# Kernel tuning notes

Hardware: AMD Instinct MI355X
Metric: run time of the kernel (lower is better)

Reference implementation:

```python
import jax, jax.numpy as jnp
import numpy as np

N = 50000   # nodes per graph
E = 400000  # edges per graph (avg degree 8)
L = 16      # regex token length per edge
V = 64      # VOCAB_SIZE
EMB = 32    # REGEX_EMBEDDING_DIMENSION
H = 128     # LSTM_DIMENSION
D = 373     # hidden_vector_dim (MAX_STATES=50)
IN_IDX = 161
OUT_IDX = 320
SID = 53    # MAX_STATES + 3
SLOPE = 0.2 # GATv2 leaky_relu negative slope

def _lstm_cell(x_t, h, c, Wih, Whh, b):
    g = x_t @ Wih.T + h @ Whh.T + b          # [E, 4H], torch gate order i,f,g,o
    i, f, gg, o = jnp.split(g, 4, axis=-1)
    c = jax.nn.sigmoid(f) * c + jax.nn.sigmoid(i) * jnp.tanh(gg)
    h = jax.nn.sigmoid(o) * jnp.tanh(c)
    return h, c

def _edge_scalar(tokens, embed, Wih_f, Whh_f, b_f, Wih_r, Whh_r, b_r, W1, b1, W2, b2):
    emb = embed.at[0].set(0.0)[tokens]       # padding_idx=0; [E, L, EMB]
    En = tokens.shape[0]
    h0 = jnp.zeros((En, H), jnp.float32)
    def step(carry, x_t):
        h, c = _lstm_cell(x_t, carry[0], carry[1], Wih_f, Whh_f, b_f)
        return (h, c), None
    (h_fwd, _), _ = jax.lax.scan(step, (h0, h0), jnp.swapaxes(emb, 0, 1))
    # bidirectional output at last timestep: reverse direction has consumed only token L-1
    h_bwd, _ = _lstm_cell(emb[:, -1], h0, h0, Wih_r, Whh_r, b_r)
    feat = jax.nn.relu(jnp.concatenate([h_fwd, h_bwd], axis=-1) @ W1 + b1)
    return jax.nn.relu(feat @ W2 + b2)[:, 0]  # [E]

def _gatv2(x, src, dst, Wl, bl, Wr, br, att, bias):
    xl = x @ Wl + bl                          # source transform (messages)
    xr = x @ Wr + br                          # target transform
    m = jax.nn.leaky_relu(xl[src] + xr[dst], SLOPE)  # [E, D]
    e = m @ att                                      # [E]
    e_max = jax.ops.segment_max(e, dst, num_segments=N)
    ex = jnp.exp(e - e_max[dst])
    denom = jax.ops.segment_sum(ex, dst, num_segments=N)
    alpha = ex / (denom[dst] + 1e-16)                # scatter-softmax over in-edges
    agg = jax.ops.segment_sum(alpha[:, None] * xl[src], dst, num_segments=N)
    return agg + bias

def _process(x, ei, edge_attr, Wl, bl, Wr, br, att, bias):
    src, dst = ei[0], ei[1]
    src_id = jnp.argmax(x[src, :SID], axis=-1)
    tgt_id = jnp.argmax(x[dst, :SID], axis=-1)
    x = x.at[dst, IN_IDX + src_id].set(edge_attr)   # index_put scatter writes
    x = x.at[src, OUT_IDX + tgt_id].set(edge_attr)
    return jax.nn.relu(_gatv2(x, src, dst, Wl, bl, Wr, br, att, bias) + x)

def setup_inputs():
    key = jax.random.key(0)
    ks = jax.random.split(key, 40)
    rn = lambda k, s, sc=0.05: jax.random.normal(k, s, dtype=jnp.float32) * sc
    return {
        "fx": jax.random.normal(ks[0], (N, D), dtype=jnp.float32),
        "bx": jax.random.normal(ks[1], (N, D), dtype=jnp.float32),
        "f_edge_index": jax.random.randint(ks[2], (2, E), 0, N),
        "b_edge_index": jax.random.randint(ks[3], (2, E), 0, N),
        "f_tokens": jax.random.randint(ks[4], (E, L), 0, V),
        "b_tokens": jax.random.randint(ks[5], (E, L), 0, V),
        "embed": rn(ks[6], (V, EMB), 1.0),
        "Wih_f": rn(ks[7], (4 * H, EMB)),
        "Whh_f": rn(ks[8], (4 * H, H)),
        "bih_f": rn(ks[9], (4 * H,)),
        "bhh_f": rn(ks[10], (4 * H,)),
        "Wih_r": rn(ks[11], (4 * H, EMB)),
        "Whh_r": rn(ks[12], (4 * H, H)),
        "bih_r": rn(ks[13], (4 * H,)),
        "bhh_r": rn(ks[14], (4 * H,)),
        "W1": rn(ks[15], (2 * H, 32)),
        "b1": rn(ks[16], (32,)),
        "W2": rn(ks[17], (32, 1)),
        "b2": rn(ks[18], (1,)),
        "fWl": rn(ks[19], (D, D)), "fbl": rn(ks[20], (D,)),
        "fWr": rn(ks[21], (D, D)), "fbr": rn(ks[22], (D,)),
        "fatt": rn(ks[23], (D,)), "fbias": rn(ks[24], (D,)),
        "bWl": rn(ks[25], (D, D)), "bbl": rn(ks[26], (D,)),
        "bWr": rn(ks[27], (D, D)), "bbr": rn(ks[28], (D,)),
        "batt": rn(ks[29], (D,)), "bbias": rn(ks[30], (D,)),
    }

def reference(fx, bx, f_edge_index, b_edge_index, f_tokens, b_tokens, embed,
              Wih_f, Whh_f, bih_f, bhh_f, Wih_r, Whh_r, bih_r, bhh_r,
              W1, b1, W2, b2,
              fWl, fbl, fWr, fbr, fatt, fbias,
              bWl, bbl, bWr, bbr, batt, bbias):
    b_f = bih_f + bhh_f
    b_r = bih_r + bhh_r
    f_ea = _edge_scalar(f_tokens, embed, Wih_f, Whh_f, b_f, Wih_r, Whh_r, b_r, W1, b1, W2, b2)
    b_ea = _edge_scalar(b_tokens, embed, Wih_f, Whh_f, b_f, Wih_r, Whh_r, b_r, W1, b1, W2, b2)
    fxo = _process(fx, f_edge_index, f_ea, fWl, fbl, fWr, fbr, fatt, fbias)
    bxo = _process(bx, b_edge_index, b_ea, bWl, bbl, bWr, bbr, batt, bbias)
    return jnp.concatenate([fxo, bxo], axis=-1)  # [N, 2*D]
```

## Files before the change

### kernel.cpp

```cpp
#include <hip/hip_runtime.h>
#include <cstdint>


#define D_DIM   373
#define SID_N   53
#define IN_COL  161
#define OUT_COL 320
#define HS_STRIDE 136
#define EDGES_T 64
#define N_ES    4

typedef short bf16x8 __attribute__((ext_vector_type(8)));
typedef float f32x4  __attribute__((ext_vector_type(4)));

#define LOG2E_F 1.4426950408889634f
#define TWO_LOG2E_F 2.8853900817779268f

__device__ __forceinline__ float fast_exp2(float x) {
#if __has_builtin(__builtin_amdgcn_exp2f)
  return __builtin_amdgcn_exp2f(x);
#else
  return exp2f(x);
#endif
}
__device__ __forceinline__ float fast_rcp(float x) {
#if __has_builtin(__builtin_amdgcn_rcpf)
  return __builtin_amdgcn_rcpf(x);
#else
  return 1.0f / x;
#endif
}
__device__ __forceinline__ float sig_ref(float x)  { return 1.0f / (1.0f + __expf(-x)); }
__device__ __forceinline__ float tanh_ref(float x) { return 2.0f / (1.0f + __expf(-2.0f * x)) - 1.0f; }

__device__ __forceinline__ unsigned short f2bf(float f) {
  unsigned u = __float_as_uint(f);
  unsigned r = (u + 0x7fffu + ((u >> 16) & 1u)) >> 16;
  return (unsigned short)r;
}
__device__ __forceinline__ float bflo2f(unsigned u) { return __uint_as_float(u << 16); }
__device__ __forceinline__ float bfhi2f(unsigned u) { return __uint_as_float(u & 0xffff0000u); }
__device__ __forceinline__ unsigned cvt_pk_bf16(float lo, float hi) {
  unsigned r;
  asm("v_cvt_pk_bf16_f32 %0, %1, %2" : "=v"(r) : "v"(lo), "v"(hi));
  return r;
}
__device__ __forceinline__ float pair_sig_tanh(float A, float B) {
  return (B - 1.0f) * fast_rcp((1.0f + A) * (1.0f + B));
}

__global__ void fill_u32_kernel(unsigned* __restrict__ p, unsigned v, size_t n) {
  size_t i = (size_t)blockIdx.x * blockDim.x + threadIdx.x;
  size_t stride = (size_t)gridDim.x * blockDim.x;
  for (; i < n; i += stride) p[i] = v;
}

__global__ void precompute_kernel(
    const float* __restrict__ embed, const float* __restrict__ Wih_f,
    const float* __restrict__ Whh_f,
    const float* __restrict__ bih_f, const float* __restrict__ bhh_f,
    const float* __restrict__ Wih_r,
    const float* __restrict__ bih_r, const float* __restrict__ bhh_r,
    const float* __restrict__ W1, const float* __restrict__ b1,
    unsigned short* __restrict__ Pg, unsigned short* __restrict__ BfragW,
    unsigned short* __restrict__ Bfrag1, float* __restrict__ FB)
{
  __shared__ float ps[512];
  __shared__ float gb[512];
  __shared__ float hb[128];
  int v = blockIdx.x;
  int j = threadIdx.x;

  float s = 0.0f;
  if (v != 0) {
    #pragma unroll
    for (int k = 0; k < 32; ++k) s += embed[v * 32 + k] * Wih_f[j * 32 + k];
  }
  ps[j] = s + bih_f[j] + bhh_f[j];

  float gr = bih_r[j] + bhh_r[j];
  if (v != 0) {
    #pragma unroll
    for (int k = 0; k < 32; ++k) gr += embed[v * 32 + k] * Wih_r[j * 32 + k];
  }
  gb[j] = gr;
  __syncthreads();
  if (j < 128) {
    float c = sig_ref(gb[j]) * tanh_ref(gb[256 + j]);
    hb[j] = sig_ref(gb[384 + j]) * tanh_ref(c);
  }
  __syncthreads();

  { int h = j >> 2, g = j & 3;
    float sc = (g == 2) ? TWO_LOG2E_F : -LOG2E_F;
    Pg[((size_t)v * 128 + h) * 4 + g] = f2bf(ps[g * 128 + h] * sc); }

  if (j < 32) {
    float s2 = b1[j];
    for (int m = 0; m < 128; ++m) s2 += hb[m] * W1[(128 + m) * 32 + j];
    FB[v * 32 + j] = s2;
  }

  if (v == 0) {
    for (int f = j; f < 65536; f += 512) {
      int e = f & 7, l = (f >> 3) & 63, ks = (f >> 9) & 3, nt = f >> 11;
      int n = nt * 16 + (l & 15);
      int k = ks * 32 + (l >> 4) * 8 + e;
      float sc = ((nt >> 3) == 2) ? TWO_LOG2E_F : -LOG2E_F;
      BfragW[f] = f2bf(Whh_f[(size_t)n * 128 + k] * sc);
    }
  }
  if (v == 1) {
    for (int f = j; f < 4096; f += 512) {
      int e = f & 7, l = (f >> 3) & 63, ks = (f >> 9) & 3, n2 = f >> 11;
      int q = n2 * 16 + (l & 15);
      int k = ks * 32 + (l >> 4) * 8 + e;
      Bfrag1[f] = f2bf(W1[(size_t)k * 32 + q]);
    }
  }
}

__global__ __launch_bounds__(512, 4) void lstm_mfma_kernel(
    const int*   __restrict__ tokens,
    const unsigned short* __restrict__ Pg,
    const unsigned short* __restrict__ BfragW,
    const unsigned short* __restrict__ Bfrag1,
    const float* __restrict__ FB,
    const float* __restrict__ W2,
    const float* __restrict__ b2,
    float* __restrict__ ea, int E, int nTiles)
{
  __shared__ unsigned short Hs[2][EDGES_T * HS_STRIDE];
  __shared__ int toks[16][EDGES_T];

  int tid  = threadIdx.x;
  int lane = tid & 63;
  int wv2  = tid >> 6;
  int l15  = lane & 15;
  int lg   = lane >> 4;
  int hbase = wv2 * 16 + lg * 4;

  bf16x8 BW[4][4];
  #pragma unroll
  for (int gate = 0; gate < 4; ++gate)
    #pragma unroll
    for (int ks = 0; ks < 4; ++ks)
      BW[gate][ks] = *(const bf16x8*)(BfragW +
          ((size_t)((gate * 8 + wv2) * 4 + ks) * 64 + lane) * 8);

  for (int tile = blockIdx.x; tile < nTiles; tile += gridDim.x) {
    int e0 = tile * EDGES_T;
    for (int i = tid; i < 16 * EDGES_T; i += 512) {
      int m = i >> 4, t = i & 15;
      int ee = e0 + m; if (ee >= E) ee = E - 1;
      toks[t][m] = tokens[(size_t)ee * 16 + t];
    }
    __syncthreads();

    f32x4 cst[N_ES];
    #pragma unroll
    for (int es = 0; es < N_ES; ++es) {
      int eL = es * 16 + l15;
      int v0 = toks[0][eL];
      const uint4* pp = (const uint4*)(Pg + ((size_t)v0 * 128 + hbase) * 4);
      uint4 pa = pp[0], pb = pp[1];
      float pi[4] = {bflo2f(pa.x), bflo2f(pa.z), bflo2f(pb.x), bflo2f(pb.z)};
      float pg[4] = {bflo2f(pa.y), bflo2f(pa.w), bflo2f(pb.y), bflo2f(pb.w)};
      float po[4] = {bfhi2f(pa.y), bfhi2f(pa.w), bfhi2f(pb.y), bfhi2f(pb.w)};
      float h[4];
      #pragma unroll
      for (int r = 0; r < 4; ++r) {
        float A = fast_exp2(pi[r]);
        float B = fast_exp2(pg[r]);
        float O = fast_exp2(po[r]);
        float cn = pair_sig_tanh(A, B);
        cst[es][r] = cn;
        float C = fast_exp2(TWO_LOG2E_F * cn);
        h[r] = pair_sig_tanh(O, C);
      }
      uint2 hp = make_uint2(cvt_pk_bf16(h[0], h[1]), cvt_pk_bf16(h[2], h[3]));
      *(uint2*)(&Hs[0][eL * HS_STRIDE + hbase]) = hp;
    }
    __syncthreads();

    int cur = 0;
    #pragma unroll 1
    for (int t = 1; t < 16; ++t) {
      #pragma unroll
      for (int es = 0; es < N_ES; ++es) {
        int eL = es * 16 + l15;
        int vt = toks[t][eL];
        const uint4* pp = (const uint4*)(Pg + ((size_t)vt * 128 + hbase) * 4);
        uint4 pa = pp[0], pb = pp[1];
        f32x4 acc[4];
        acc[0] = (f32x4){bflo2f(pa.x), bflo2f(pa.z), bflo2f(pb.x), bflo2f(pb.z)};
        acc[1] = (f32x4){bfhi2f(pa.x), bfhi2f(pa.z), bfhi2f(pb.x), bfhi2f(pb.z)};
        acc[2] = (f32x4){bflo2f(pa.y), bflo2f(pa.w), bflo2f(pb.y), bflo2f(pb.w)};
        acc[3] = (f32x4){bfhi2f(pa.y), bfhi2f(pa.w), bfhi2f(pb.y), bfhi2f(pb.w)};

        #pragma unroll
        for (int ks = 0; ks < 4; ++ks) {
          bf16x8 Hf = *(const bf16x8*)(&Hs[cur][eL * HS_STRIDE + ks * 32 + lg * 8]);
          #pragma unroll
          for (int gate = 0; gate < 4; ++gate)
            acc[gate] = __builtin_amdgcn_mfma_f32_16x16x32_bf16(
                BW[gate][ks], Hf, acc[gate], 0, 0, 0);
        }

        float h[4];
        #pragma unroll
        for (int r = 0; r < 4; ++r) {
          float A = fast_exp2(acc[0][r]);
          float F = fast_exp2(acc[1][r]);
          float B = fast_exp2(acc[2][r]);
          float O = fast_exp2(acc[3][r]);
          float ig = pair_sig_tanh(A, B);
          float f  = fast_rcp(1.0f + F);
          float cn = fmaf(f, cst[es][r], ig);
          cst[es][r] = cn;
          float C = fast_exp2(TWO_LOG2E_F * cn);
          h[r] = pair_sig_tanh(O, C);
        }
        uint2 hp = make_uint2(cvt_pk_bf16(h[0], h[1]), cvt_pk_bf16(h[2], h[3]));
        *(uint2*)(&Hs[cur ^ 1][eL * HS_STRIDE + hbase]) = hp;
      }
      cur ^= 1;
      __syncthreads();
    }

    if (wv2 < N_ES) {
      int eL = wv2 * 16 + l15;
      bf16x8 Hf[4];
      #pragma unroll
      for (int ks = 0; ks < 4; ++ks)
        Hf[ks] = *(const bf16x8*)(&Hs[cur][eL * HS_STRIDE + ks * 32 + lg * 8]);
      f32x4 a2[2];
      a2[0] = (f32x4){0.f, 0.f, 0.f, 0.f};
      a2[1] = (f32x4){0.f, 0.f, 0.f, 0.f};
      #pragma unroll
      for (int ks = 0; ks < 4; ++ks)
        #pragma unroll
        for (int n2 = 0; n2 < 2; ++n2)
          a2[n2] = __builtin_amdgcn_mfma_f32_16x16x32_bf16(
              *(const bf16x8*)(Bfrag1 + ((size_t)(n2 * 4 + ks) * 64 + lane) * 8),
              Hf[ks], a2[n2], 0, 0, 0);
      float4 w2lo = *(const float4*)(W2 + lg * 4);
      float4 w2hi = *(const float4*)(W2 + 16 + lg * 4);
      float b2v = b2[0];
      int v15 = toks[15][eL];
      float4 fb0 = *(const float4*)(FB + v15 * 32 + lg * 4);
      float4 fb1 = *(const float4*)(FB + v15 * 32 + 16 + lg * 4);
      float pr = fmaxf(a2[0][0] + fb0.x, 0.f) * w2lo.x
               + fmaxf(a2[0][1] + fb0.y, 0.f) * w2lo.y
               + fmaxf(a2[0][2] + fb0.z, 0.f) * w2lo.z
               + fmaxf(a2[0][3] + fb0.w, 0.f) * w2lo.w
               + fmaxf(a2[1][0] + fb1.x, 0.f) * w2hi.x
               + fmaxf(a2[1][1] + fb1.y, 0.f) * w2hi.y
               + fmaxf(a2[1][2] + fb1.z, 0.f) * w2hi.z
               + fmaxf(a2[1][3] + fb1.w, 0.f) * w2hi.w;
      pr += __shfl_xor(pr, 16);
      pr += __shfl_xor(pr, 32);
      int eidx = e0 + eL;
      if (lane < 16 && eidx < E) ea[eidx] = fmaxf(pr + b2v, 0.0f);
    }
    __syncthreads();
  }
}

__global__ __launch_bounds__(256) void node_argmax_kernel(
    const float* __restrict__ x, int* __restrict__ nid, int N)
{
  int n = (blockIdx.x * 256 + threadIdx.x) >> 6;
  int lane = threadIdx.x & 63;
  if (n >= N) return;
  float v = (lane < SID_N) ? x[(size_t)n * D_DIM + lane] : -3.4e38f;
  int idx = lane;
  #pragma unroll
  for (int o = 32; o > 0; o >>= 1) {
    float ov = __shfl_down(v, o);
    int   oi = __shfl_down(idx, o);
    if (ov > v || (ov == v && oi < idx)) { v = ov; idx = oi; }
  }
  if (lane == 0) nid[n] = idx;
}

__global__ void edge_winner_kernel(
    const int* __restrict__ ei, const int* __restrict__ nid,
    int* __restrict__ win_in, int* __restrict__ win_out, int E)
{
  int e = blockIdx.x * 256 + threadIdx.x;
  if (e >= E) return;
  int s = ei[e];
  int t = ei[E + e];
  atomicMax(&win_in[(size_t)t * SID_N + nid[s]], e);
  atomicMax(&win_out[(size_t)s * SID_N + nid[t]], e);
}

__global__ void scatter_resolve_kernel(
    const int* __restrict__ ei, const int* __restrict__ nid,
    const float* __restrict__ ea,
    const int* __restrict__ win_in, const int* __restrict__ win_out,
    float* __restrict__ x_mod, int E)
{
  int e = blockIdx.x * 256 + threadIdx.x;
  if (e >= E) return;
  int s = ei[e];
  int t = ei[E + e];
  int sid = nid[s], tix = nid[t];
  if (win_in[(size_t)t * SID_N + sid] == e)
    x_mod[(size_t)t * D_DIM + IN_COL + sid] = ea[e];
  if (win_out[(size_t)s * SID_N + tix] == e)
    x_mod[(size_t)s * D_DIM + OUT_COL + tix] = ea[e];
}

__global__ void pack_w_kernel(const float* __restrict__ Wl,
                              const float* __restrict__ Wr,
                              unsigned short* __restrict__ Wfrag)
{
  int f = blockIdx.x * 256 + threadIdx.x;
  if (f >= 48 * 12 * 64 * 8) return;
  int e = f & 7, l = (f >> 3) & 63;
  int rest = f >> 9;
  int ks = rest % 12, nt = rest / 12;
  int nl = nt * 16 + (l & 15);
  int k  = ks * 32 + (l >> 4) * 8 + e;
  float val = 0.0f;
  if (k < D_DIM) {
    if (nl < D_DIM)                      val = Wl[(size_t)k * D_DIM + nl];
    else if (nl >= 384 && nl < 384 + D_DIM) val = Wr[(size_t)k * D_DIM + (nl - 384)];
  }
  Wfrag[f] = f2bf(val);
}

__global__ __launch_bounds__(256, 2) void gemm_mfma_kernel(
    const float* __restrict__ A,
    const unsigned short* __restrict__ Wfrag,
    const float* __restrict__ bl, const float* __restrict__ br,
    float* __restrict__ xl, float* __restrict__ xr, int N)
{
  __shared__ unsigned short As[64][40];
  int tid  = threadIdx.x;
  int lane = tid & 63;
  int wv   = tid >> 6;
  int l15  = lane & 15, lg = lane >> 4;
  int m0   = blockIdx.x * 64;
  int nt   = blockIdx.y * 4 + wv;

  f32x4 acc[4];
  #pragma unroll
  for (int i = 0; i < 4; ++i) acc[i] = (f32x4){0.f, 0.f, 0.f, 0.f};

  int srow = tid >> 2, seg = tid & 3;
  int gr = m0 + srow; if (gr >= N) gr = N - 1;
  const float* arow = A + (size_t)gr * D_DIM;

  for (int ks = 0; ks < 12; ++ks) {
    int c0 = ks * 32 + seg * 8;
    float v[8];
    #pragma unroll
    for (int j = 0; j < 8; ++j) v[j] = (c0 + j < D_DIM) ? arow[c0 + j] : 0.0f;
    unsigned pk0 = cvt_pk_bf16(v[0], v[1]);
    unsigned pk1 = cvt_pk_bf16(v[2], v[3]);
    unsigned pk2 = cvt_pk_bf16(v[4], v[5]);
    unsigned pk3 = cvt_pk_bf16(v[6], v[7]);
    __syncthreads();
    *(uint4*)(&As[srow][seg * 8]) = make_uint4(pk0, pk1, pk2, pk3);
    __syncthreads();

    bf16x8 Bf = *(const bf16x8*)(Wfrag + ((size_t)(nt * 12 + ks) * 64 + lane) * 8);
    #pragma unroll
    for (int msub = 0; msub < 4; ++msub) {
      bf16x8 Af = *(const bf16x8*)(&As[msub * 16 + l15][lg * 8]);
      acc[msub] = __builtin_amdgcn_mfma_f32_16x16x32_bf16(Af, Bf, acc[msub], 0, 0, 0);
    }
  }

  int nl = nt * 16 + l15;
  float* dst = nullptr; int col = 0; const float* bias_ = nullptr;
  if (nl < D_DIM)                         { dst = xl; col = nl;       bias_ = bl; }
  else if (nl >= 384 && nl < 384 + D_DIM) { dst = xr; col = nl - 384; bias_ = br; }
  if (dst) {
    float bv = bias_[col];
    #pragma unroll
    for (int msub = 0; msub < 4; ++msub) {
      #pragma unroll
      for (int r = 0; r < 4; ++r) {
        int m = m0 + msub * 16 + lg * 4 + r;
        if (m < N) dst[(size_t)m * D_DIM + col] = acc[msub][r] + bv;
      }
    }
  }
}

__global__ __launch_bounds__(256) void edge_e_kernel(
    const float* __restrict__ xl, const float* __restrict__ xr,
    const float* __restrict__ att, const int* __restrict__ ei,
    float* __restrict__ e_buf, int E)
{
  int widx = (blockIdx.x * 256 + threadIdx.x) >> 6;
  int lane = threadIdx.x & 63;
  if (widx >= E) return;
  int s = ei[widx], t = ei[E + widx];
  const float* pl = xl + (size_t)s * D_DIM;
  const float* pr = xr + (size_t)t * D_DIM;
  float acc = 0.0f;
  for (int d = lane; d < D_DIM; d += 64) {
    float m = pl[d] + pr[d];
    m = (m > 0.0f) ? m : 0.2f * m;
    acc += m * att[d];
  }
  #pragma unroll
  for (int o = 32; o > 0; o >>= 1) acc += __shfl_down(acc, o);
  if (lane == 0) e_buf[widx] = acc;
}

__global__ void hist_kernel(const int* __restrict__ ei, unsigned* __restrict__ deg,
                            int E) {
  int e = blockIdx.x * 256 + threadIdx.x;
  if (e >= E) return;
  atomicAdd(&deg[ei[E + e]], 1u);
}

__global__ void scan1_kernel(const unsigned* __restrict__ deg,
                             unsigned* __restrict__ excl,
                             unsigned* __restrict__ bsum, int n) {
  __shared__ unsigned s[256];
  int t = threadIdx.x;
  int i = blockIdx.x * 256 + t;
  unsigned v = (i < n) ? deg[i] : 0u;
  s[t] = v; __syncthreads();
  #pragma unroll
  for (int o = 1; o < 256; o <<= 1) {
    unsigned u = (t >= o) ? s[t - o] : 0u;
    __syncthreads();
    s[t] += u;
    __syncthreads();
  }
  if (i < n) excl[i] = s[t] - v;
  if (t == 255) bsum[blockIdx.x] = s[255];
}

__global__ void scan2_kernel(unsigned* __restrict__ bsum, int nb) {
  __shared__ unsigned s[256];
  int t = threadIdx.x;
  unsigned v = (t < nb) ? bsum[t] : 0u;
  s[t] = v; __syncthreads();
  #pragma unroll
  for (int o = 1; o < 256; o <<= 1) {
    unsigned u = (t >= o) ? s[t - o] : 0u;
    __syncthreads();
    s[t] += u;
    __syncthreads();
  }
  if (t < nb) bsum[t] = s[t] - v;
}

__global__ void scan3_kernel(unsigned* __restrict__ excl,
                             const unsigned* __restrict__ bsum, int n) {
  int i = blockIdx.x * 256 + threadIdx.x;
  if (i < n) excl[i] += bsum[i >> 8];
}

__global__ void place_kernel(const int* __restrict__ ei,
                             unsigned* __restrict__ offs,
                             int* __restrict__ csr_eid, int E) {
  int e = blockIdx.x * 256 + threadIdx.x;
  if (e >= E) return;
  unsigned j = atomicAdd(&offs[ei[E + e]], 1u);
  csr_eid[j] = e;
}

__global__ __launch_bounds__(256) void node_gat_kernel(
    const int* __restrict__ ei, const int* __restrict__ csr_eid,
    const unsigned* __restrict__ offs, const unsigned* __restrict__ deg,
    float* __restrict__ ebuf, const float* __restrict__ xl,
    const float* __restrict__ xmod, const float* __restrict__ bias,
    float* __restrict__ out, int N, int E, int goff)
{
  int n = (blockIdx.x * 256 + threadIdx.x) >> 6;
  int lane = threadIdx.x & 63;
  if (n >= N) return;
  unsigned end = offs[n], d = deg[n], start = end - d;

  float mx = -3.4e38f;
  for (unsigned j = start; j < end; ++j)
    mx = fmaxf(mx, ebuf[csr_eid[j]]);
  float den = 0.0f;
  for (unsigned j = start; j < end; ++j) {
    int eid = csr_eid[j];
    float ex = __expf(ebuf[eid] - mx);
    ebuf[eid] = ex;
    den += ex;
  }
  float inv = 1.0f / (den + 1e-16f);

  float o0 = 0, o1 = 0, o2 = 0, o3 = 0, o4 = 0, o5 = 0;
  for (unsigned j = start; j < end; ++j) {
    int eid = csr_eid[j];
    float w = ebuf[eid] * inv;
    const float* row = xl + (size_t)ei[eid] * D_DIM;
    o0 = fmaf(w, row[lane], o0);
    o1 = fmaf(w, row[64 + lane], o1);
    o2 = fmaf(w, row[128 + lane], o2);
    o3 = fmaf(w, row[192 + lane], o3);
    o4 = fmaf(w, row[256 + lane], o4);
    if (lane < 53) o5 = fmaf(w, row[320 + lane], o5);
  }

  const float* xm = xmod + (size_t)n * D_DIM;
  float* op = out + (size_t)n * (2 * D_DIM) + goff;
  op[lane]       = fmaxf(o0 + bias[lane]       + xm[lane],       0.0f);
  op[64 + lane]  = fmaxf(o1 + bias[64 + lane]  + xm[64 + lane],  0.0f);
  op[128 + lane] = fmaxf(o2 + bias[128 + lane] + xm[128 + lane], 0.0f);
  op[192 + lane] = fmaxf(o3 + bias[192 + lane] + xm[192 + lane], 0.0f);
  op[256 + lane] = fmaxf(o4 + bias[256 + lane] + xm[256 + lane], 0.0f);
  if (lane < 53)
    op[320 + lane] = fmaxf(o5 + bias[320 + lane] + xm[320 + lane], 0.0f);
}

extern "C" void kernel_launch(void* const* d_in, const int* in_sizes, int n_in,
                              void* d_out, int out_size, void* d_ws, size_t ws_size,
                              hipStream_t stream)
{
  const float* fx     = (const float*)d_in[0];
  const float* bx     = (const float*)d_in[1];
  const int*   fei    = (const int*)d_in[2];
  const int*   bei    = (const int*)d_in[3];
  const int*   ftk    = (const int*)d_in[4];
  const int*   btk    = (const int*)d_in[5];
  const float* embed  = (const float*)d_in[6];
  const float* Wih_f  = (const float*)d_in[7];
  const float* Whh_f  = (const float*)d_in[8];
  const float* bih_f  = (const float*)d_in[9];
  const float* bhh_f  = (const float*)d_in[10];
  const float* Wih_r  = (const float*)d_in[11];
  const float* bih_r  = (const float*)d_in[13];
  const float* bhh_r  = (const float*)d_in[14];
  const float* W1     = (const float*)d_in[15];
  const float* b1     = (const float*)d_in[16];
  const float* W2     = (const float*)d_in[17];
  const float* b2     = (const float*)d_in[18];

  const float* Wl_g[2]   = {(const float*)d_in[19], (const float*)d_in[25]};
  const float* bl_g[2]   = {(const float*)d_in[20], (const float*)d_in[26]};
  const float* Wr_g[2]   = {(const float*)d_in[21], (const float*)d_in[27]};
  const float* br_g[2]   = {(const float*)d_in[22], (const float*)d_in[28]};
  const float* att_g[2]  = {(const float*)d_in[23], (const float*)d_in[29]};
  const float* bias_g[2] = {(const float*)d_in[24], (const float*)d_in[30]};
  const float* x_g[2]    = {fx, bx};
  const int*   ei_g[2]   = {fei, bei};
  const int*   tk_g[2]   = {ftk, btk};

  const int E = in_sizes[2] / 2;
  const int N = in_sizes[0] / D_DIM;

  char* wsb = (char*)d_ws;
  size_t off = 0;
  auto alloc = [&](size_t bytes) -> void* {
    void* p = wsb + off; off += (bytes + 255) & ~(size_t)255; return p;
  };
  unsigned short* Pg     = (unsigned short*)alloc((size_t)64 * 128 * 4 * 2);
  unsigned short* BfragW = (unsigned short*)alloc((size_t)65536 * 2);
  unsigned short* Bfrag1 = (unsigned short*)alloc((size_t)4096 * 2);
  unsigned short* Wfrag2 = (unsigned short*)alloc((size_t)2 * 294912 * 2);
  float* FB    = (float*)alloc((size_t)64 * 32 * 4);
  float* ea    = (float*)alloc((size_t)E * 4);
  float* ebuf  = (float*)alloc((size_t)E * 4);
  int*   nid   = (int*)alloc((size_t)N * 4);
  int*   csr_eid = (int*)alloc((size_t)E * 4);
  unsigned* deg  = (unsigned*)alloc((size_t)N * 4);
  unsigned* offs = (unsigned*)alloc((size_t)N * 4);
  unsigned* bsum = (unsigned*)alloc((size_t)256 * 4);
  int* win_in  = (int*)alloc((size_t)N * SID_N * 4);
  int* win_out = (int*)alloc((size_t)N * SID_N * 4);
  float* xmod  = (float*)alloc((size_t)N * D_DIM * 4);
  float* xl    = (float*)alloc((size_t)N * D_DIM * 4);
  float* xr    = (float*)alloc((size_t)N * D_DIM * 4);
  (void)ws_size; (void)n_in; (void)out_size;

  const size_t win_u32 = (size_t)((char*)win_out - (char*)win_in) / 4
                         + (size_t)N * SID_N;

  float* out = (float*)d_out;

  precompute_kernel<<<64, 512, 0, stream>>>(
      embed, Wih_f, Whh_f, bih_f, bhh_f, Wih_r, bih_r, bhh_r, W1, b1,
      Pg, BfragW, Bfrag1, FB);
  pack_w_kernel<<<(294912 + 255) / 256, 256, 0, stream>>>(
      Wl_g[0], Wr_g[0], Wfrag2);
  pack_w_kernel<<<(294912 + 255) / 256, 256, 0, stream>>>(
      Wl_g[1], Wr_g[1], Wfrag2 + 294912);

  const int nTiles  = (E + EDGES_T - 1) / EDGES_T;
  const int gridL   = nTiles < 2048 ? nTiles : 2048;
  const int gridE   = (E + 255) / 256;
  const int gridEW  = (E + 3) / 4;
  const int nScanB  = (N + 255) / 256;
  const int gridNd  = (N * 64 + 255) / 256;
  dim3 gridG((N + 63) / 64, 12);

  for (int g = 0; g < 2; ++g) {
    const float* x  = x_g[g];
    const int*   ei = ei_g[g];

    lstm_mfma_kernel<<<gridL, 512, 0, stream>>>(tk_g[g], Pg, BfragW, Bfrag1,
                                                FB, W2, b2, ea, E, nTiles);

    hipMemcpyAsync(xmod, x, (size_t)N * D_DIM * sizeof(float),
                   hipMemcpyDeviceToDevice, stream);
    node_argmax_kernel<<<gridNd, 256, 0, stream>>>(x, nid, N);
    fill_u32_kernel<<<2048, 256, 0, stream>>>((unsigned*)win_in, 0xFFFFFFFFu,
                                              win_u32);
    edge_winner_kernel<<<gridE, 256, 0, stream>>>(ei, nid, win_in, win_out, E);
    scatter_resolve_kernel<<<gridE, 256, 0, stream>>>(ei, nid, ea,
                                                      win_in, win_out, xmod, E);

    gemm_mfma_kernel<<<gridG, 256, 0, stream>>>(xmod, Wfrag2 + (size_t)g * 294912,
                                                bl_g[g], br_g[g], xl, xr, N);

    fill_u32_kernel<<<512, 256, 0, stream>>>(deg, 0u, (size_t)N);
    hist_kernel<<<gridE, 256, 0, stream>>>(ei, deg, E);
    scan1_kernel<<<nScanB, 256, 0, stream>>>(deg, offs, bsum, N);
    scan2_kernel<<<1, 256, 0, stream>>>(bsum, nScanB);
    scan3_kernel<<<nScanB, 256, 0, stream>>>(offs, bsum, N);
    place_kernel<<<gridE, 256, 0, stream>>>(ei, offs, csr_eid, E);

    edge_e_kernel<<<gridEW, 256, 0, stream>>>(xl, xr, att_g[g], ei, ebuf, E);
    node_gat_kernel<<<gridNd, 256, 0, stream>>>(ei, csr_eid, offs, deg, ebuf,
                                                xl, xmod, bias_g[g], out,
                                                N, E, g * D_DIM);
  }
}
```

Before: 3.596 ms.

## Compute GAT edge scores per destination node via CSR, reuse target row

Replaces the per-edge attention-score kernel with a per-node kernel that walks each node's in-edges through the CSR. The target row xr[n] and the att vector are loaded into registers once per node instead of once per edge, cutting global reads. It also shrinks the LSTM edge tile from 64 to 48 edges (N_ES 4 to 3), which changes that kernel's occupancy and grid size. The cost is serial work per node, so load balance depends on the degree distribution.

Result: faster. 3.525 ms (-2.0%).

```diff
diff --git a/kernel.cpp b/kernel.cpp
--- a/kernel.cpp
+++ b/kernel.cpp
@@ -7,8 +7,8 @@
 #define IN_COL  161
 #define OUT_COL 320
 #define HS_STRIDE 136
-#define EDGES_T 64
-#define N_ES    4
+#define EDGES_T 48
+#define N_ES    3
 
 typedef short bf16x8 __attribute__((ext_vector_type(8)));
 typedef float f32x4  __attribute__((ext_vector_type(4)));
@@ -392,28 +392,6 @@
   }
 }
 
-__global__ __launch_bounds__(256) void edge_e_kernel(
-    const float* __restrict__ xl, const float* __restrict__ xr,
-    const float* __restrict__ att, const int* __restrict__ ei,
-    float* __restrict__ e_buf, int E)
-{
-  int widx = (blockIdx.x * 256 + threadIdx.x) >> 6;
-  int lane = threadIdx.x & 63;
-  if (widx >= E) return;
-  int s = ei[widx], t = ei[E + widx];
-  const float* pl = xl + (size_t)s * D_DIM;
-  const float* pr = xr + (size_t)t * D_DIM;
-  float acc = 0.0f;
-  for (int d = lane; d < D_DIM; d += 64) {
-    float m = pl[d] + pr[d];
-    m = (m > 0.0f) ? m : 0.2f * m;
-    acc += m * att[d];
-  }
-  #pragma unroll
-  for (int o = 32; o > 0; o >>= 1) acc += __shfl_down(acc, o);
-  if (lane == 0) e_buf[widx] = acc;
-}
-
 __global__ void hist_kernel(const int* __restrict__ ei, unsigned* __restrict__ deg,
                             int E) {
   int e = blockIdx.x * 256 + threadIdx.x;
@@ -468,6 +446,43 @@
   if (e >= E) return;
   unsigned j = atomicAdd(&offs[ei[E + e]], 1u);
   csr_eid[j] = e;
+}
+
+__global__ __launch_bounds__(256) void edge_e_csr_kernel(
+    const float* __restrict__ xl, const float* __restrict__ xr,
+    const float* __restrict__ att, const int* __restrict__ ei,
+    const int* __restrict__ csr_eid, const unsigned* __restrict__ offs,
+    const unsigned* __restrict__ deg, float* __restrict__ ebuf, int N, int E)
+{
+  int n = (blockIdx.x * 256 + threadIdx.x) >> 6;
+  int lane = threadIdx.x & 63;
+  if (n >= N) return;
+  unsigned end = offs[n], d = deg[n], start = end - d;
+  if (d == 0) return;
+
+  const float* xrn = xr + (size_t)n * D_DIM;
+  float r0 = xrn[lane],        a0 = att[lane];
+  float r1 = xrn[64 + lane],   a1 = att[64 + lane];
+  float r2 = xrn[128 + lane],  a2 = att[128 + lane];
+  float r3 = xrn[192 + lane],  a3 = att[192 + lane];
+  float r4 = xrn[256 + lane],  a4 = att[256 + lane];
+  float r5 = 0.f, a5 = 0.f;
+  if (lane < 53) { r5 = xrn[320 + lane]; a5 = att[320 + lane]; }
+
+  for (unsigned j = start; j < end; ++j) {
+    int eid = csr_eid[j];
+    const float* row = xl + (size_t)ei[eid] * D_DIM;
+    float m, acc;
+    m = row[lane] + r0;        acc  = ((m > 0.f) ? m : 0.2f * m) * a0;
+    m = row[64 + lane] + r1;   acc += ((m > 0.f) ? m : 0.2f * m) * a1;
+    m = row[128 + lane] + r2;  acc += ((m > 0.f) ? m : 0.2f * m) * a2;
+    m = row[192 + lane] + r3;  acc += ((m > 0.f) ? m : 0.2f * m) * a3;
+    m = row[256 + lane] + r4;  acc += ((m > 0.f) ? m : 0.2f * m) * a4;
+    if (lane < 53) { m = row[320 + lane] + r5; acc += ((m > 0.f) ? m : 0.2f * m) * a5; }
+    #pragma unroll
+    for (int o = 32; o > 0; o >>= 1) acc += __shfl_down(acc, o);
+    if (lane == 0) ebuf[eid] = acc;
+  }
 }
 
 __global__ __launch_bounds__(256) void node_gat_kernel(
@@ -594,7 +609,6 @@
   const int nTiles  = (E + EDGES_T - 1) / EDGES_T;
   const int gridL   = nTiles < 2048 ? nTiles : 2048;
   const int gridE   = (E + 255) / 256;
-  const int gridEW  = (E + 3) / 4;
   const int nScanB  = (N + 255) / 256;
   const int gridNd  = (N * 64 + 255) / 256;
   dim3 gridG((N + 63) / 64, 12);
@@ -625,7 +639,8 @@
     scan3_kernel<<<nScanB, 256, 0, stream>>>(offs, bsum, N);
     place_kernel<<<gridE, 256, 0, stream>>>(ei, offs, csr_eid, E);
 
-    edge_e_kernel<<<gridEW, 256, 0, stream>>>(xl, xr, att_g[g], ei, ebuf, E);
+    edge_e_csr_kernel<<<gridNd, 256, 0, stream>>>(xl, xr, att_g[g], ei,
+                                                  csr_eid, offs, deg, ebuf, N, E);
     node_gat_kernel<<<gridNd, 256, 0, stream>>>(ei, csr_eid, offs, deg, ebuf,
                                                 xl, xmod, bias_g[g], out,
                                                 N, E, g * D_DIM);
```
